# Performance work log

Measured on AMD Instinct MI355X. Metric: run time of the kernel, lower is better.

Reference implementation:

```python
import jax, jax.numpy as jnp
import numpy as np

B, T, I, H = 256, 2000, 23, 128


def setup_inputs() -> dict:
    key = jax.random.key(0)
    ks = jax.random.split(key, 5)
    s = 1.0 / np.sqrt(H)  # PyTorch GRU init bound
    return {
        "x": jax.random.normal(ks[0], (B, T, I), dtype=jnp.float32),
        "W_ih": jax.random.uniform(ks[1], (3 * H, I), jnp.float32, -s, s),
        "W_hh": jax.random.uniform(ks[2], (3 * H, H), jnp.float32, -s, s),
        "b_ih": jax.random.uniform(ks[3], (3 * H,), jnp.float32, -s, s),
        "b_hh": jax.random.uniform(ks[4], (3 * H,), jnp.float32, -s, s),
    }


def reference(x, W_ih, W_hh, b_ih, b_hh):
    """Single-layer unidirectional GRU (PyTorch gate order r,z,n),
    followed by mean over time. Dropout is identity (eval mode)."""
    Bb, Tt, _ = x.shape
    Hh = W_hh.shape[1]
    # Precompute input-side gate projections for all timesteps: [T, B, 3H]
    gx = jnp.einsum('bti,gi->tbg', x, W_ih) + b_ih

    def step(h, g):
        gh = h @ W_hh.T + b_hh                               # [B, 3H]
        r = jax.nn.sigmoid(g[:, :Hh] + gh[:, :Hh])
        z = jax.nn.sigmoid(g[:, Hh:2 * Hh] + gh[:, Hh:2 * Hh])
        n = jnp.tanh(g[:, 2 * Hh:] + r * gh[:, 2 * Hh:])
        h_new = (1.0 - z) * n + z * h
        return h_new, h_new

    h0 = jnp.zeros((Bb, Hh), dtype=x.dtype)
    _, hs = jax.lax.scan(step, h0, gx)                       # hs: [T, B, H]
    return jnp.mean(hs, axis=0)                              # [B, H]
```

## Files before the change

### kernel.cpp

```cpp
#include <hip/hip_runtime.h>


#define Bb 256
#define Tt 2000
#define Ii 23
#define Hh 128

typedef float v2f __attribute__((ext_vector_type(2)));
typedef float v4f __attribute__((ext_vector_type(4)));

template <int N> struct ic { static constexpr int v = N; };

template <int ctrl>
__device__ __forceinline__ float dpp_movf(float v) {
    int r = __builtin_amdgcn_update_dpp(0, __builtin_bit_cast(int, v),
                                        ctrl, 0xf, 0xf, true);
    return __builtin_bit_cast(float, r);
}
__device__ __forceinline__ void pk_fma(v2f& a, v2f b, v2f c) {
    asm("v_pk_fma_f32 %0, %1, %2, %0" : "+v"(a) : "v"(b), "v"(c));
}
__device__ __forceinline__ v2f pk_mul(v2f b, v2f c) {
    v2f d;
    asm("v_pk_mul_f32 %0, %1, %2" : "=v"(d) : "v"(b), "v"(c));
    return d;
}
__device__ __forceinline__ float fexp2(float x) {
#if __has_builtin(__builtin_amdgcn_exp2f)
    return __builtin_amdgcn_exp2f(x);
#else
    return exp2f(x);
#endif
}
__device__ __forceinline__ v2f pinv(v2f v) { asm("" : "+v"(v)); return v; }
__device__ __forceinline__ float pinf(float v) { asm("" : "+v"(v)); return v; }
__device__ __forceinline__ void bar_lds() {
    asm volatile("s_waitcnt lgkmcnt(0)\n\ts_barrier" ::: "memory");
}
__device__ __forceinline__ float qfold(float c) {
    c += dpp_movf<0xB1>(c);
    c += dpp_movf<0x4E>(c);
    return c;
}

__global__ __launch_bounds__(512, 2)
void gru_fused(const float* __restrict__ x,
               const float* __restrict__ W_ih,
               const float* __restrict__ W_hh,
               const float* __restrict__ b_ih,
               const float* __restrict__ b_hh,
               float* __restrict__ out)
{
    const int b   = blockIdx.x;
    const int tid = threadIdx.x;
    const int wid = tid >> 6;
    const int l   = tid & 63;
    const int jj  = l >> 2;
    const int kt  = l & 3;
    const int j   = wid * 16 + jj;
    const int kb  = kt * 32;

    __shared__ __align__(16) float h_db[2][4][36];

    const float L2E = 1.4426950408889634f;
    const float K2  = 2.0f * L2E;

    v2f wr[16], wz[16], wn[16];
    {
        const float* Wr = W_hh + (size_t)j * Hh + kb;
        const float* Wz = W_hh + (size_t)(Hh + j) * Hh + kb;
        const float* Wn = W_hh + (size_t)(2 * Hh + j) * Hh + kb;
        #pragma unroll
        for (int kk = 0; kk < 16; ++kk) {
            v2f a = *reinterpret_cast<const v2f*>(Wr + 2 * kk);
            a[0] *= L2E; a[1] *= L2E; wr[kk] = pinv(a);
            v2f c = *reinterpret_cast<const v2f*>(Wz + 2 * kk);
            c[0] *= L2E; c[1] *= L2E; wz[kk] = pinv(c);
            v2f d = *reinterpret_cast<const v2f*>(Wn + 2 * kk);
            d[0] *= K2;  d[1] *= K2;  wn[kk] = pinv(d);
        }
    }

    const int xi0 = (kt < 3) ? kt * 6 : 18;
    const int xo2 = (kt < 3) ? 4 : 3;
    v2f wxr[3], wxz[3], wxn[3];
    {
        const float* Xr = W_ih + (size_t)j * Ii;
        const float* Xz = W_ih + (size_t)(Hh + j) * Ii;
        const float* Xn = W_ih + (size_t)(2 * Hh + j) * Ii;
        #pragma unroll
        for (int m = 0; m < 3; ++m) {
            const int e0 = xi0 + ((m < 2) ? 2 * m : xo2);
            const float klo = (kt == 3 && m == 2) ? 0.0f : 1.0f;
            v2f a; a[0] = Xr[e0] * L2E * klo; a[1] = Xr[e0 + 1] * L2E;
            wxr[m] = pinv(a);
            v2f c; c[0] = Xz[e0] * L2E * klo; c[1] = Xz[e0 + 1] * L2E;
            wxz[m] = pinv(c);
            v2f d; d[0] = Xn[e0] * K2 * klo;  d[1] = Xn[e0 + 1] * K2;
            wxn[m] = pinv(d);
        }
    }

    const float br  = pinf((b_ih[j] + b_hh[j]) * L2E);
    const float bz  = pinf((b_ih[Hh + j] + b_hh[Hh + j]) * L2E);
    const float bnh = pinf(b_hh[2 * Hh + j] * K2);
    const float bnx = pinf(b_ih[2 * Hh + j] * K2);

    const float* xrow = x + (size_t)b * Tt * Ii + xi0;

    if (tid < Hh) h_db[0][tid >> 5][tid & 31] = 0.0f;
    float xA[6], xB[6];
    {
        #pragma unroll
        for (int m = 0; m < 4; ++m) { xA[m] = xrow[m]; xB[m] = xrow[Ii + m]; }
        xA[4] = xrow[xo2];     xA[5] = xrow[xo2 + 1];
        xB[4] = xrow[Ii + xo2]; xB[5] = xrow[Ii + xo2 + 1];
    }
    int xob = 2 * Ii;
    float h_prev = 0.0f, acc_mean = 0.0f;
    bar_lds();

    auto body = [&](auto CUR, int s) {
        constexpr int cur = decltype(CUR)::v;
        const int step = s + cur;

        v2f xp0, xp1, xp2;
        if constexpr (cur == 0) {
            xp0[0]=xA[0]; xp0[1]=xA[1]; xp1[0]=xA[2]; xp1[1]=xA[3];
            xp2[0]=xA[4]; xp2[1]=xA[5];
        } else {
            xp0[0]=xB[0]; xp0[1]=xB[1]; xp1[0]=xB[2]; xp1[1]=xB[3];
            xp2[0]=xB[4]; xp2[1]=xB[5];
        }
        v2f ar = pk_mul(wxr[0], xp0);
        pk_fma(ar, wxr[1], xp1); pk_fma(ar, wxr[2], xp2);
        v2f az = pk_mul(wxz[0], xp0);
        pk_fma(az, wxz[1], xp1); pk_fma(az, wxz[2], xp2);
        v2f ax = pk_mul(wxn[0], xp0);
        pk_fma(ax, wxn[1], xp1); pk_fma(ax, wxn[2], xp2);

        v2f ah;
        #pragma unroll
        for (int c = 0; c < 8; ++c) {
            const v4f hc = *reinterpret_cast<const v4f*>(&h_db[cur][kt][4 * c]);
            const v2f hpA = __builtin_shufflevector(hc, hc, 0, 1);
            const v2f hpB = __builtin_shufflevector(hc, hc, 2, 3);
            pk_fma(ar, wr[2 * c], hpA); pk_fma(ar, wr[2 * c + 1], hpB);
            pk_fma(az, wz[2 * c], hpA); pk_fma(az, wz[2 * c + 1], hpB);
            if (c == 0) {
                ah = pk_mul(wn[0], hpA); pk_fma(ah, wn[1], hpB);
            } else {
                pk_fma(ah, wn[2 * c], hpA); pk_fma(ah, wn[2 * c + 1], hpB);
            }
        }

        if constexpr (cur == 0) {
            #pragma unroll
            for (int m = 0; m < 4; ++m) xA[m] = xrow[xob + m];
            xA[4] = xrow[xob + xo2]; xA[5] = xrow[xob + xo2 + 1];
        } else {
            #pragma unroll
            for (int m = 0; m < 4; ++m) xB[m] = xrow[xob + m];
            xB[4] = xrow[xob + xo2]; xB[5] = xrow[xob + xo2 + 1];
        }
        if (step + 3 < Tt) xob += Ii;

        const float r_s = qfold(ar[0] + ar[1]) + br;
        const float z_s = qfold(az[0] + az[1]) + bz;
        const float ghn = qfold(ah[0] + ah[1]) + bnh;
        const float gxn = qfold(ax[0] + ax[1]) + bnx;

        const float r  = __builtin_amdgcn_rcpf(1.0f + fexp2(-r_s));
        const float z  = __builtin_amdgcn_rcpf(1.0f + fexp2(-z_s));
        const float npre = fmaf(r, ghn, gxn);
        const float tt2  = __builtin_amdgcn_rcpf(1.0f + fexp2(-npre));
        const float nn   = fmaf(2.0f, tt2, -1.0f);
        const float h_new = fmaf(z, h_prev - nn, nn);
        h_prev = h_new;
        acc_mean += h_new;
        if (kt == 0) h_db[cur ^ 1][j >> 5][j & 31] = h_new;
        bar_lds();
    };

    for (int s = 0; s < Tt; s += 2) {
        body(ic<0>{}, s);
        body(ic<1>{}, s);
    }

    if (kt == 0) out[(size_t)b * Hh + j] = acc_mean * (1.0f / Tt);
}

extern "C" void kernel_launch(void* const* d_in, const int* in_sizes, int n_in,
                              void* d_out, int out_size, void* d_ws, size_t ws_size,
                              hipStream_t stream) {
    const float* x    = (const float*)d_in[0];
    const float* W_ih = (const float*)d_in[1];
    const float* W_hh = (const float*)d_in[2];
    const float* b_ih = (const float*)d_in[3];
    const float* b_hh = (const float*)d_in[4];
    float* out = (float*)d_out;

    gru_fused<<<Bb, 512, 0, stream>>>(x, W_ih, W_hh, b_ih, b_hh, out);
}
```

Before: 1.020 ms.

## Split each hidden unit's K reduction across 8 lanes with 1024-thread blocks

New measurement: 1.291 ms. +26.5%, slower.

```diff
diff --git a/kernel.cpp b/kernel.cpp
--- a/kernel.cpp
+++ b/kernel.cpp
@@ -8,6 +8,7 @@
 
 typedef float v2f __attribute__((ext_vector_type(2)));
 typedef float v4f __attribute__((ext_vector_type(4)));
+typedef float v4fu __attribute__((ext_vector_type(4), aligned(4)));
 
 template <int N> struct ic { static constexpr int v = N; };
 
@@ -37,13 +38,14 @@
 __device__ __forceinline__ void bar_lds() {
     asm volatile("s_waitcnt lgkmcnt(0)\n\ts_barrier" ::: "memory");
 }
-__device__ __forceinline__ float qfold(float c) {
+__device__ __forceinline__ float ofold(float c) {
     c += dpp_movf<0xB1>(c);
     c += dpp_movf<0x4E>(c);
+    c += dpp_movf<0x128>(c);
     return c;
 }
 
-__global__ __launch_bounds__(512, 2)
+__global__ __launch_bounds__(1024, 4)
 void gru_fused(const float* __restrict__ x,
                const float* __restrict__ W_ih,
                const float* __restrict__ W_hh,
@@ -55,23 +57,23 @@
     const int tid = threadIdx.x;
     const int wid = tid >> 6;
     const int l   = tid & 63;
-    const int jj  = l >> 2;
-    const int kt  = l & 3;
-    const int j   = wid * 16 + jj;
-    const int kb  = kt * 32;
+    const int kt  = (l & 3) | ((l & 8) >> 1);
+    const int jj  = ((l & 4) >> 2) | ((l & 48) >> 3);
+    const int j   = wid * 8 + jj;
+    const int kb  = kt * 16;
 
-    __shared__ __align__(16) float h_db[2][4][36];
+    __shared__ __align__(16) float h_db[2][8][20];
 
     const float L2E = 1.4426950408889634f;
     const float K2  = 2.0f * L2E;
 
-    v2f wr[16], wz[16], wn[16];
+    v2f wr[8], wz[8], wn[8];
     {
         const float* Wr = W_hh + (size_t)j * Hh + kb;
         const float* Wz = W_hh + (size_t)(Hh + j) * Hh + kb;
         const float* Wn = W_hh + (size_t)(2 * Hh + j) * Hh + kb;
         #pragma unroll
-        for (int kk = 0; kk < 16; ++kk) {
+        for (int kk = 0; kk < 8; ++kk) {
             v2f a = *reinterpret_cast<const v2f*>(Wr + 2 * kk);
             a[0] *= L2E; a[1] *= L2E; wr[kk] = pinv(a);
             v2f c = *reinterpret_cast<const v2f*>(Wz + 2 * kk);
@@ -81,24 +83,21 @@
         }
     }
 
-    const int xi0 = (kt < 3) ? kt * 6 : 18;
-    const int xo2 = (kt < 3) ? 4 : 3;
-    v2f wxr[3], wxz[3], wxn[3];
+    const int e0x = (kt < 7) ? 3 * kt : 19;
+    const float m0 = (kt < 7) ? 1.0f : 0.0f;
+    const float m3 = (kt < 7) ? 0.0f : 1.0f;
+    v2f wxr[2], wxz[2], wxn[2];
     {
-        const float* Xr = W_ih + (size_t)j * Ii;
-        const float* Xz = W_ih + (size_t)(Hh + j) * Ii;
-        const float* Xn = W_ih + (size_t)(2 * Hh + j) * Ii;
-        #pragma unroll
-        for (int m = 0; m < 3; ++m) {
-            const int e0 = xi0 + ((m < 2) ? 2 * m : xo2);
-            const float klo = (kt == 3 && m == 2) ? 0.0f : 1.0f;
-            v2f a; a[0] = Xr[e0] * L2E * klo; a[1] = Xr[e0 + 1] * L2E;
-            wxr[m] = pinv(a);
-            v2f c; c[0] = Xz[e0] * L2E * klo; c[1] = Xz[e0 + 1] * L2E;
-            wxz[m] = pinv(c);
-            v2f d; d[0] = Xn[e0] * K2 * klo;  d[1] = Xn[e0 + 1] * K2;
-            wxn[m] = pinv(d);
-        }
+        const float* Xr = W_ih + (size_t)j * Ii + e0x;
+        const float* Xz = W_ih + (size_t)(Hh + j) * Ii + e0x;
+        const float* Xn = W_ih + (size_t)(2 * Hh + j) * Ii + e0x;
+        v2f t;
+        t[0] = Xr[0] * L2E * m0; t[1] = Xr[1] * L2E * m0; wxr[0] = pinv(t);
+        t[0] = Xr[2] * L2E;      t[1] = Xr[3] * L2E * m3; wxr[1] = pinv(t);
+        t[0] = Xz[0] * L2E * m0; t[1] = Xz[1] * L2E * m0; wxz[0] = pinv(t);
+        t[0] = Xz[2] * L2E;      t[1] = Xz[3] * L2E * m3; wxz[1] = pinv(t);
+        t[0] = Xn[0] * K2 * m0;  t[1] = Xn[1] * K2 * m0;  wxn[0] = pinv(t);
+        t[0] = Xn[2] * K2;       t[1] = Xn[3] * K2 * m3;  wxn[1] = pinv(t);
     }
 
     const float br  = pinf((b_ih[j] + b_hh[j]) * L2E);
@@ -106,16 +105,11 @@
     const float bnh = pinf(b_hh[2 * Hh + j] * K2);
     const float bnx = pinf(b_ih[2 * Hh + j] * K2);
 
-    const float* xrow = x + (size_t)b * Tt * Ii + xi0;
+    const float* xptr = x + (size_t)b * Tt * Ii + e0x;
 
-    if (tid < Hh) h_db[0][tid >> 5][tid & 31] = 0.0f;
-    float xA[6], xB[6];
-    {
-        #pragma unroll
-        for (int m = 0; m < 4; ++m) { xA[m] = xrow[m]; xB[m] = xrow[Ii + m]; }
-        xA[4] = xrow[xo2];     xA[5] = xrow[xo2 + 1];
-        xB[4] = xrow[Ii + xo2]; xB[5] = xrow[Ii + xo2 + 1];
-    }
+    if (tid < Hh) h_db[0][tid >> 4][tid & 15] = 0.0f;
+    v4f qA = *reinterpret_cast<const v4fu*>(xptr);
+    v4f qB = *reinterpret_cast<const v4fu*>(xptr + Ii);
     int xob = 2 * Ii;
     float h_prev = 0.0f, acc_mean = 0.0f;
     bar_lds();
@@ -124,27 +118,22 @@
         constexpr int cur = decltype(CUR)::v;
         const int step = s + cur;
 
-        v2f xp0, xp1, xp2;
+        v2f xp0, xp1;
         if constexpr (cur == 0) {
-            xp0[0]=xA[0]; xp0[1]=xA[1]; xp1[0]=xA[2]; xp1[1]=xA[3];
-            xp2[0]=xA[4]; xp2[1]=xA[5];
+            xp0[0] = qA[0]; xp0[1] = qA[1]; xp1[0] = qA[2]; xp1[1] = qA[3];
         } else {
-            xp0[0]=xB[0]; xp0[1]=xB[1]; xp1[0]=xB[2]; xp1[1]=xB[3];
-            xp2[0]=xB[4]; xp2[1]=xB[5];
+            xp0[0] = qB[0]; xp0[1] = qB[1]; xp1[0] = qB[2]; xp1[1] = qB[3];
         }
-        v2f ar = pk_mul(wxr[0], xp0);
-        pk_fma(ar, wxr[1], xp1); pk_fma(ar, wxr[2], xp2);
-        v2f az = pk_mul(wxz[0], xp0);
-        pk_fma(az, wxz[1], xp1); pk_fma(az, wxz[2], xp2);
-        v2f ax = pk_mul(wxn[0], xp0);
-        pk_fma(ax, wxn[1], xp1); pk_fma(ax, wxn[2], xp2);
+        v2f ar = pk_mul(wxr[0], xp0); pk_fma(ar, wxr[1], xp1);
+        v2f az = pk_mul(wxz[0], xp0); pk_fma(az, wxz[1], xp1);
+        v2f ax = pk_mul(wxn[0], xp0); pk_fma(ax, wxn[1], xp1);
 
         v2f ah;
         #pragma unroll
-        for (int c = 0; c < 8; ++c) {
+        for (int c = 0; c < 4; ++c) {
             const v4f hc = *reinterpret_cast<const v4f*>(&h_db[cur][kt][4 * c]);
-            const v2f hpA = __builtin_shufflevector(hc, hc, 0, 1);
-            const v2f hpB = __builtin_shufflevector(hc, hc, 2, 3);
+            v2f hpA; hpA[0] = hc[0]; hpA[1] = hc[1];
+            v2f hpB; hpB[0] = hc[2]; hpB[1] = hc[3];
             pk_fma(ar, wr[2 * c], hpA); pk_fma(ar, wr[2 * c + 1], hpB);
             pk_fma(az, wz[2 * c], hpA); pk_fma(az, wz[2 * c + 1], hpB);
             if (c == 0) {
@@ -154,21 +143,14 @@
             }
         }
 
-        if constexpr (cur == 0) {
-            #pragma unroll
-            for (int m = 0; m < 4; ++m) xA[m] = xrow[xob + m];
-            xA[4] = xrow[xob + xo2]; xA[5] = xrow[xob + xo2 + 1];
-        } else {
-            #pragma unroll
-            for (int m = 0; m < 4; ++m) xB[m] = xrow[xob + m];
-            xB[4] = xrow[xob + xo2]; xB[5] = xrow[xob + xo2 + 1];
-        }
+        if constexpr (cur == 0) qA = *reinterpret_cast<const v4fu*>(xptr + xob);
+        else                    qB = *reinterpret_cast<const v4fu*>(xptr + xob);
         if (step + 3 < Tt) xob += Ii;
 
-        const float r_s = qfold(ar[0] + ar[1]) + br;
-        const float z_s = qfold(az[0] + az[1]) + bz;
-        const float ghn = qfold(ah[0] + ah[1]) + bnh;
-        const float gxn = qfold(ax[0] + ax[1]) + bnx;
+        const float r_s = ofold(ar[0] + ar[1]) + br;
+        const float z_s = ofold(az[0] + az[1]) + bz;
+        const float ghn = ofold(ah[0] + ah[1]) + bnh;
+        const float gxn = ofold(ax[0] + ax[1]) + bnx;
 
         const float r  = __builtin_amdgcn_rcpf(1.0f + fexp2(-r_s));
         const float z  = __builtin_amdgcn_rcpf(1.0f + fexp2(-z_s));
@@ -178,7 +160,7 @@
         const float h_new = fmaf(z, h_prev - nn, nn);
         h_prev = h_new;
         acc_mean += h_new;
-        if (kt == 0) h_db[cur ^ 1][j >> 5][j & 31] = h_new;
+        if (kt == 0) h_db[cur ^ 1][j >> 4][j & 15] = h_new;
         bar_lds();
     };
 
@@ -200,5 +182,5 @@
     const float* b_hh = (const float*)d_in[4];
     float* out = (float*)d_out;
 
-    gru_fused<<<Bb, 512, 0, stream>>>(x, W_ih, W_hh, b_ih, b_hh, out);
+    gru_fused<<<Bb, 1024, 0, stream>>>(x, W_ih, W_hh, b_ih, b_hh, out);
 }
```
